# Kernel optimization log

Hardware: AMD Instinct MI355X
Metric: run time of the kernel (lower is better)

Reference implementation:

```python
import jax, jax.numpy as jnp
import numpy as np

NUM_ENTITIES = 100000
NUM_RELATIONS = 1000
ENTITY_DIM = 256
RELATION_DIM = 256
BATCH = 8192


def setup_inputs() -> dict:
    key = jax.random.key(0)
    k1, k2, k3, k4, k5, k6 = jax.random.split(key, 6)
    bound_e = 6.0 / np.sqrt(ENTITY_DIM)
    bound_r = 6.0 / np.sqrt(RELATION_DIM)
    entity_embed = jax.random.uniform(k1, (NUM_ENTITIES, ENTITY_DIM), jnp.float32, -bound_e, bound_e)
    relation_embed = jax.random.uniform(k2, (NUM_RELATIONS, RELATION_DIM), jnp.float32, -bound_r, bound_r)
    # proj matrices initialized near identity (TransR convention) plus small noise
    eye = jnp.broadcast_to(jnp.eye(RELATION_DIM, ENTITY_DIM, dtype=jnp.float32), (NUM_RELATIONS, RELATION_DIM, ENTITY_DIM))
    proj = (eye + 0.01 * jax.random.normal(k3, (NUM_RELATIONS, RELATION_DIM, ENTITY_DIM), jnp.float32)).reshape(NUM_RELATIONS, RELATION_DIM * ENTITY_DIM)
    h = jax.random.randint(k4, (BATCH,), 0, NUM_ENTITIES)
    r = jax.random.randint(k5, (BATCH,), 0, NUM_RELATIONS)
    t = jax.random.randint(k6, (BATCH,), 0, NUM_ENTITIES)
    return {"h": h, "r": r, "t": t, "entity_embed": entity_embed,
            "relation_embed": relation_embed, "proj": proj}


def reference(h, r, t, entity_embed, relation_embed, proj) -> jnp.ndarray:
    # gather embeddings
    h_emb = entity_embed[h]                      # [B, ed]
    t_emb = entity_embed[t]                      # [B, ed]
    r_emb = relation_embed[r]                    # [B, rd]
    M = proj[r].reshape(-1, RELATION_DIM, ENTITY_DIM)  # [B, rd, ed]
    # batched matvec: project head/tail into relation space
    h_r = jnp.einsum('bre,be->br', M, h_emb)     # [B, rd]
    t_r = jnp.einsum('bre,be->br', M, t_emb)     # [B, rd]
    diff = h_r + r_emb - t_r
    return -jnp.sqrt(jnp.sum(diff * diff, axis=-1))  # [B]
```

## Files before the change

kernel.cpp:

```cpp
#include <hip/hip_runtime.h>
#include <math.h>


#define ED   256
#define TR64 64
#define NT   4
#define CAP  64

typedef __attribute__((ext_vector_type(8))) short bf16x8;
typedef __attribute__((ext_vector_type(4))) float f32x4;

__device__ __forceinline__ unsigned int bfbits_rne(float x) {
    unsigned int u = __builtin_bit_cast(unsigned int, x);
    return (u + 0x7fffu + ((u >> 16) & 1u)) >> 16;
}
__device__ __forceinline__ unsigned int pack2(float x, float y) {
    return bfbits_rne(x) | (bfbits_rne(y) << 16);
}

__global__ void transr_prep_kernel(const int* __restrict__ h, const int* __restrict__ r,
                                   const int* __restrict__ t, const float* __restrict__ ent,
                                   int B, int nbCsr,
                                   int* __restrict__ counts, int* __restrict__ itemsG,
                                   uint4* __restrict__ Dbf)
{
    const int tid = threadIdx.x;
    if ((int)blockIdx.x < nbCsr) {
        int i = blockIdx.x * 256 + tid;
        if (i < B) {
            int rv  = r[i];
            int pos = atomicAdd(&counts[rv], 1);
            if (pos < CAP) itemsG[rv * CAP + pos] = i;
        }
    } else {
        int i = ((int)blockIdx.x - nbCsr) * 256 + tid;
        if (i < B * 32) {
            int b = i >> 5, c = i & 31;
            const float4* hv = (const float4*)ent + (size_t)h[b] * 64 + c * 2;
            const float4* tv = (const float4*)ent + (size_t)t[b] * 64 + c * 2;
            float4 a0 = hv[0], a1 = hv[1], b0 = tv[0], b1 = tv[1];
            uint4 o;
            o.x = pack2(a0.x - b0.x, a0.y - b0.y);
            o.y = pack2(a0.z - b0.z, a0.w - b0.w);
            o.z = pack2(a1.x - b1.x, a1.y - b1.y);
            o.w = pack2(a1.z - b1.z, a1.w - b1.w);
            Dbf[i] = o;
        }
    }
}

__global__ __launch_bounds__(256, 2)
void transr_mfma_kernel(const float* __restrict__ rel, const float* __restrict__ proj,
                        const int* __restrict__ counts, const int* __restrict__ itemsG,
                        const uint4* __restrict__ Dbf, float* __restrict__ part)
{
    __shared__ __align__(16) unsigned short Mt[TR64 * ED];
    __shared__ __align__(16) unsigned short Dt[16 * ED];
    __shared__ float remb_s[TR64];
    __shared__ float sacc[4][16];
    __shared__ int   items_s[CAP];

    const int relid = blockIdx.x;
    const int tile  = blockIdx.y;
    const int tid   = threadIdx.x;

    const int n = min(counts[relid], CAP);
    if (n == 0) return;

    if (tid < CAP) items_s[tid] = (tid < n) ? itemsG[relid * CAP + tid] : 0;
    if (tid < TR64) remb_s[tid] = rel[(size_t)relid * ED + tile * TR64 + tid];

    {
        const float4* Mg4 = (const float4*)(proj + (size_t)relid * ED * ED
                                                 + (size_t)tile * TR64 * ED);
        #pragma unroll
        for (int it = 0; it < 8; ++it) {
            int f  = tid + 256 * it;
            int rr = f >> 5, c = f & 31;
            float4 a = Mg4[2 * f], b = Mg4[2 * f + 1];
            uint4 o;
            o.x = pack2(a.x, a.y); o.y = pack2(a.z, a.w);
            o.z = pack2(b.x, b.y); o.w = pack2(b.z, b.w);
            *(uint4*)&Mt[rr * ED + ((c ^ (rr & 7)) << 3)] = o;
        }
    }

    const int l  = tid & 63;
    const int w  = tid >> 6;
    const int li = l & 15;
    const int lk = l >> 4;
    const int arow = w * 16 + li;
    const int aswz = arow & 7, bswz = li & 7;

    for (int c0 = 0; c0 < n; c0 += 16) {
        #pragma unroll
        for (int it = 0; it < 2; ++it) {
            int f = tid + 256 * it;
            int j = f >> 5, c = f & 31;
            uint4 v = {0u, 0u, 0u, 0u};
            if (c0 + j < n) v = Dbf[(size_t)items_s[c0 + j] * 32 + c];
            *(uint4*)&Dt[j * ED + ((c ^ (j & 7)) << 3)] = v;
        }
        __syncthreads();

        f32x4 acc = {0.f, 0.f, 0.f, 0.f};
        #pragma unroll
        for (int kk = 0; kk < 8; ++kk) {
            int c = kk * 4 + lk;
            bf16x8 av = *(const bf16x8*)&Mt[arow * ED + ((c ^ aswz) << 3)];
            bf16x8 bv = *(const bf16x8*)&Dt[li * ED + ((c ^ bswz) << 3)];
            acc = __builtin_amdgcn_mfma_f32_16x16x32_bf16(av, bv, acc, 0, 0, 0);
        }

        float s = 0.f;
        #pragma unroll
        for (int j = 0; j < 4; ++j) {
            float v = acc[j] + remb_s[w * 16 + lk * 4 + j];
            s = fmaf(v, v, s);
        }
        s += __shfl_xor(s, 16);
        s += __shfl_xor(s, 32);
        if (l < 16) sacc[w][l] = s;
        __syncthreads();

        if (tid < 16 && c0 + tid < n) {
            part[(size_t)items_s[c0 + tid] * NT + tile] =
                sacc[0][tid] + sacc[1][tid] + sacc[2][tid] + sacc[3][tid];
        }
    }
}

__global__ void transr_finalize_kernel(const float* __restrict__ part,
                                       float* __restrict__ out, int B)
{
    int i = blockIdx.x * 256 + threadIdx.x;
    if (i < B) {
        float4 p = *(const float4*)(part + (size_t)i * NT);
        out[i] = -sqrtf(p.x + p.y + p.z + p.w);
    }
}

#define FNCH 16
#define FCAP 2048
__global__ __launch_bounds__(256, 1)
void transr_score_kernel(const int* __restrict__ h, const int* __restrict__ r,
                         const int* __restrict__ t, const float* __restrict__ ent,
                         const float* __restrict__ rel, const float* __restrict__ proj,
                         float* __restrict__ out, int B)
{
    __shared__ int   items[FCAP];
    __shared__ int   s_n;
    __shared__ __align__(16) float D[FNCH][ED];
    __shared__ __align__(16) float Mt2[32][ED];
    __shared__ float remb[ED];
    __shared__ float sacc2[FNCH];

    const int relid = blockIdx.x;
    const int tid   = threadIdx.x;
    if (tid == 0) s_n = 0;
    __syncthreads();

    for (int i0 = tid * 4; i0 < B; i0 += 256 * 4) {
        int4 rv = *(const int4*)(r + i0);
        if (rv.x == relid) { int p = atomicAdd(&s_n, 1); if (p < FCAP) items[p] = i0;     }
        if (rv.y == relid) { int p = atomicAdd(&s_n, 1); if (p < FCAP) items[p] = i0 + 1; }
        if (rv.z == relid) { int p = atomicAdd(&s_n, 1); if (p < FCAP) items[p] = i0 + 2; }
        if (rv.w == relid) { int p = atomicAdd(&s_n, 1); if (p < FCAP) items[p] = i0 + 3; }
    }
    remb[tid] = rel[(size_t)relid * ED + tid];
    __syncthreads();

    int n = s_n < FCAP ? s_n : FCAP;
    if (n == 0) return;

    const float* Mg = proj + (size_t)relid * (ED * ED);
    const int rt = tid & 31, g = tid >> 5, sw = rt & 7;

    for (int c0 = 0; c0 < n; c0 += FNCH) {
        const int nc = min(FNCH, n - c0);
        {
            const int j  = tid >> 4;
            const int e4 = tid & 15;
            if (j < nc) {
                const int b = items[c0 + j];
                const float4* hv = (const float4*)(ent + (size_t)h[b] * ED);
                const float4* tv = (const float4*)(ent + (size_t)t[b] * ED);
                #pragma unroll
                for (int k = 0; k < 4; ++k) {
                    float4 a = hv[e4 + 16 * k];
                    float4 c = tv[e4 + 16 * k];
                    float4 d4; d4.x = a.x - c.x; d4.y = a.y - c.y;
                               d4.z = a.z - c.z; d4.w = a.w - c.w;
                    *(float4*)&D[j][4 * (e4 + 16 * k)] = d4;
                }
            } else {
                float4 z; z.x = z.y = z.z = z.w = 0.f;
                #pragma unroll
                for (int k = 0; k < 4; ++k) *(float4*)&D[j][4 * (e4 + 16 * k)] = z;
            }
        }
        __syncthreads();

        float sq0 = 0.f, sq1 = 0.f;
        for (int tile = 0; tile < 8; ++tile) {
            const float4* Mg4 = (const float4*)(Mg + (size_t)tile * 32 * ED);
            #pragma unroll
            for (int k = 0; k < 8; ++k) {
                int f = tid + 256 * k;
                int rr = f >> 6, e4 = f & 63;
                *(float4*)&Mt2[rr][4 * (e4 ^ (rr & 7))] = Mg4[f];
            }
            __syncthreads();

            float acc0 = 0.f, acc1 = 0.f;
            #pragma unroll 8
            for (int e4 = 0; e4 < 64; ++e4) {
                float4 m  = *(const float4*)&Mt2[rt][4 * (e4 ^ sw)];
                float4 d0 = *(const float4*)&D[g][4 * e4];
                float4 d1 = *(const float4*)&D[g + 8][4 * e4];
                acc0 = fmaf(m.x, d0.x, acc0); acc0 = fmaf(m.y, d0.y, acc0);
                acc0 = fmaf(m.z, d0.z, acc0); acc0 = fmaf(m.w, d0.w, acc0);
                acc1 = fmaf(m.x, d1.x, acc1); acc1 = fmaf(m.y, d1.y, acc1);
                acc1 = fmaf(m.z, d1.z, acc1); acc1 = fmaf(m.w, d1.w, acc1);
            }
            const float rb = remb[tile * 32 + rt];
            float s0 = acc0 + rb; s0 *= s0;
            float s1 = acc1 + rb; s1 *= s1;
            #pragma unroll
            for (int off = 16; off >= 1; off >>= 1) {
                s0 += __shfl_xor(s0, off, 32);
                s1 += __shfl_xor(s1, off, 32);
            }
            sq0 += s0; sq1 += s1;
            __syncthreads();
        }
        if (rt == 0) { sacc2[g] = sq0; sacc2[g + 8] = sq1; }
        __syncthreads();
        if (tid < nc) out[items[c0 + tid]] = -sqrtf(sacc2[tid]);
        __syncthreads();
    }
}

extern "C" void kernel_launch(void* const* d_in, const int* in_sizes, int n_in,
                              void* d_out, int out_size, void* d_ws, size_t ws_size,
                              hipStream_t stream)
{
    const int*   h    = (const int*)d_in[0];
    const int*   r    = (const int*)d_in[1];
    const int*   t    = (const int*)d_in[2];
    const float* ent  = (const float*)d_in[3];
    const float* rel  = (const float*)d_in[4];
    const float* proj = (const float*)d_in[5];
    float*       out  = (float*)d_out;

    const int B  = in_sizes[0];
    const int NR = in_sizes[5] / (ED * ED);

    size_t o_counts = 0;
    size_t o_items  = (o_counts + (size_t)NR * 4 + 255) & ~(size_t)255;
    size_t o_part   = (o_items + (size_t)NR * CAP * 4 + 255) & ~(size_t)255;
    size_t o_D      = (o_part + (size_t)B * NT * 4 + 255) & ~(size_t)255;
    size_t need     = o_D + (size_t)B * ED * 2;

    if (ws_size >= need) {
        int*   counts = (int*)((char*)d_ws + o_counts);
        int*   itemsG = (int*)((char*)d_ws + o_items);
        float* part   = (float*)((char*)d_ws + o_part);
        uint4* Dbf    = (uint4*)((char*)d_ws + o_D);

        hipMemsetAsync(counts, 0, (size_t)NR * 4, stream);

        const int nbCsr = (B + 255) / 256;
        const int nbD   = (B * 32 + 255) / 256;
        transr_prep_kernel<<<nbCsr + nbD, 256, 0, stream>>>(h, r, t, ent, B, nbCsr,
                                                            counts, itemsG, Dbf);
        transr_mfma_kernel<<<dim3(NR, NT), 256, 0, stream>>>(rel, proj, counts,
                                                             itemsG, Dbf, part);
        transr_finalize_kernel<<<(B + 255) / 256, 256, 0, stream>>>(part, out, B);
    } else {
        transr_score_kernel<<<NR, 256, 0, stream>>>(h, r, t, ent, rel, proj, out, B);
    }
}
```

Measured before the change: 62.97 us.

## Bucket batch items per relation in-block and read D directly from global

Drops the memset and the global atomic CSR bucketing. Each MFMA block now scans the whole r array itself and collects its relation's items in shared memory. The B operand is loaded straight from global memory instead of being staged in LDS, which removes the per-chunk syncthreads. Per-wave partial sums are written out and reduced in finalize, and occupancy rises to 4 blocks per CU. The cost is that each of the NR*NT blocks reads all of r (redundant traffic) and the partial buffer grows fourfold.

```diff
diff --git a/kernel.cpp b/kernel.cpp
--- a/kernel.cpp
+++ b/kernel.cpp
@@ -18,57 +18,52 @@
     return bfbits_rne(x) | (bfbits_rne(y) << 16);
 }
 
-__global__ void transr_prep_kernel(const int* __restrict__ h, const int* __restrict__ r,
-                                   const int* __restrict__ t, const float* __restrict__ ent,
-                                   int B, int nbCsr,
-                                   int* __restrict__ counts, int* __restrict__ itemsG,
+__global__ void transr_prep_kernel(const int* __restrict__ h, const int* __restrict__ t,
+                                   const float* __restrict__ ent, int B,
                                    uint4* __restrict__ Dbf)
 {
-    const int tid = threadIdx.x;
-    if ((int)blockIdx.x < nbCsr) {
-        int i = blockIdx.x * 256 + tid;
-        if (i < B) {
-            int rv  = r[i];
-            int pos = atomicAdd(&counts[rv], 1);
-            if (pos < CAP) itemsG[rv * CAP + pos] = i;
-        }
-    } else {
-        int i = ((int)blockIdx.x - nbCsr) * 256 + tid;
-        if (i < B * 32) {
-            int b = i >> 5, c = i & 31;
-            const float4* hv = (const float4*)ent + (size_t)h[b] * 64 + c * 2;
-            const float4* tv = (const float4*)ent + (size_t)t[b] * 64 + c * 2;
-            float4 a0 = hv[0], a1 = hv[1], b0 = tv[0], b1 = tv[1];
-            uint4 o;
-            o.x = pack2(a0.x - b0.x, a0.y - b0.y);
-            o.y = pack2(a0.z - b0.z, a0.w - b0.w);
-            o.z = pack2(a1.x - b1.x, a1.y - b1.y);
-            o.w = pack2(a1.z - b1.z, a1.w - b1.w);
-            Dbf[i] = o;
-        }
-    }
-}
-
-__global__ __launch_bounds__(256, 2)
-void transr_mfma_kernel(const float* __restrict__ rel, const float* __restrict__ proj,
-                        const int* __restrict__ counts, const int* __restrict__ itemsG,
-                        const uint4* __restrict__ Dbf, float* __restrict__ part)
+    int i = blockIdx.x * 256 + threadIdx.x;
+    if (i < B * 32) {
+        int b = i >> 5, c = i & 31;
+        const float4* hv = (const float4*)ent + (size_t)h[b] * 64 + c * 2;
+        const float4* tv = (const float4*)ent + (size_t)t[b] * 64 + c * 2;
+        float4 a0 = hv[0], a1 = hv[1], b0 = tv[0], b1 = tv[1];
+        uint4 o;
+        o.x = pack2(a0.x - b0.x, a0.y - b0.y);
+        o.y = pack2(a0.z - b0.z, a0.w - b0.w);
+        o.z = pack2(a1.x - b1.x, a1.y - b1.y);
+        o.w = pack2(a1.z - b1.z, a1.w - b1.w);
+        Dbf[i] = o;
+    }
+}
+
+__global__ __launch_bounds__(256, 4)
+void transr_mfma_kernel(const int* __restrict__ r, const float* __restrict__ rel,
+                        const float* __restrict__ proj, const uint4* __restrict__ Dbf,
+                        float* __restrict__ part, int B)
 {
     __shared__ __align__(16) unsigned short Mt[TR64 * ED];
-    __shared__ __align__(16) unsigned short Dt[16 * ED];
-    __shared__ float remb_s[TR64];
-    __shared__ float sacc[4][16];
-    __shared__ int   items_s[CAP];
+    __shared__ int items_s[CAP];
+    __shared__ int s_n;
 
     const int relid = blockIdx.x;
     const int tile  = blockIdx.y;
     const int tid   = threadIdx.x;
 
-    const int n = min(counts[relid], CAP);
+    if (tid == 0) s_n = 0;
+    __syncthreads();
+
+    for (int i0 = tid * 4; i0 < B; i0 += 1024) {
+        int4 rv = *(const int4*)(r + i0);
+        if (rv.x == relid) { int p = atomicAdd(&s_n, 1); if (p < CAP) items_s[p] = i0;     }
+        if (rv.y == relid) { int p = atomicAdd(&s_n, 1); if (p < CAP) items_s[p] = i0 + 1; }
+        if (rv.z == relid) { int p = atomicAdd(&s_n, 1); if (p < CAP) items_s[p] = i0 + 2; }
+        if (rv.w == relid) { int p = atomicAdd(&s_n, 1); if (p < CAP) items_s[p] = i0 + 3; }
+    }
+    __syncthreads();
+
+    const int n = min(s_n, CAP);
     if (n == 0) return;
-
-    if (tid < CAP) items_s[tid] = (tid < n) ? itemsG[relid * CAP + tid] : 0;
-    if (tid < TR64) remb_s[tid] = rel[(size_t)relid * ED + tile * TR64 + tid];
 
     {
         const float4* Mg4 = (const float4*)(proj + (size_t)relid * ED * ED
@@ -85,48 +80,40 @@
         }
     }
 
-    const int l  = tid & 63;
-    const int w  = tid >> 6;
-    const int li = l & 15;
-    const int lk = l >> 4;
+    const int l    = tid & 63;
+    const int w    = tid >> 6;
+    const int li   = l & 15;
+    const int lk   = l >> 4;
     const int arow = w * 16 + li;
-    const int aswz = arow & 7, bswz = li & 7;
+    const int aswz = arow & 7;
+
+    f32x4 rbv = *(const f32x4*)(rel + (size_t)relid * ED + tile * TR64 + w * 16 + lk * 4);
+
+    __syncthreads();
 
     for (int c0 = 0; c0 < n; c0 += 16) {
-        #pragma unroll
-        for (int it = 0; it < 2; ++it) {
-            int f = tid + 256 * it;
-            int j = f >> 5, c = f & 31;
-            uint4 v = {0u, 0u, 0u, 0u};
-            if (c0 + j < n) v = Dbf[(size_t)items_s[c0 + j] * 32 + c];
-            *(uint4*)&Dt[j * ED + ((c ^ (j & 7)) << 3)] = v;
-        }
-        __syncthreads();
+        const int bslot = min(c0 + li, n - 1);
+        const uint4* bbase = Dbf + (size_t)items_s[bslot] * 32;
 
         f32x4 acc = {0.f, 0.f, 0.f, 0.f};
         #pragma unroll
         for (int kk = 0; kk < 8; ++kk) {
             int c = kk * 4 + lk;
             bf16x8 av = *(const bf16x8*)&Mt[arow * ED + ((c ^ aswz) << 3)];
-            bf16x8 bv = *(const bf16x8*)&Dt[li * ED + ((c ^ bswz) << 3)];
+            bf16x8 bv = __builtin_bit_cast(bf16x8, bbase[c]);
             acc = __builtin_amdgcn_mfma_f32_16x16x32_bf16(av, bv, acc, 0, 0, 0);
         }
 
         float s = 0.f;
         #pragma unroll
         for (int j = 0; j < 4; ++j) {
-            float v = acc[j] + remb_s[w * 16 + lk * 4 + j];
+            float v = acc[j] + rbv[j];
             s = fmaf(v, v, s);
         }
         s += __shfl_xor(s, 16);
         s += __shfl_xor(s, 32);
-        if (l < 16) sacc[w][l] = s;
-        __syncthreads();
-
-        if (tid < 16 && c0 + tid < n) {
-            part[(size_t)items_s[c0 + tid] * NT + tile] =
-                sacc[0][tid] + sacc[1][tid] + sacc[2][tid] + sacc[3][tid];
-        }
+        if (lk == 0 && c0 + li < n)
+            part[(size_t)items_s[c0 + li] * 16 + tile * 4 + w] = s;
     }
 }
 
@@ -135,8 +122,13 @@
 {
     int i = blockIdx.x * 256 + threadIdx.x;
     if (i < B) {
-        float4 p = *(const float4*)(part + (size_t)i * NT);
-        out[i] = -sqrtf(p.x + p.y + p.z + p.w);
+        const float4* p = (const float4*)(part + (size_t)i * 16);
+        float4 a = p[0], b = p[1], c = p[2], d = p[3];
+        float s = a.x + a.y + a.z + a.w;
+        s += b.x + b.y + b.z + b.w;
+        s += c.x + c.y + c.z + c.w;
+        s += d.x + d.y + d.z + d.w;
+        out[i] = -sqrtf(s);
     }
 }
 
@@ -256,26 +248,16 @@
     const int B  = in_sizes[0];
     const int NR = in_sizes[5] / (ED * ED);
 
-    size_t o_counts = 0;
-    size_t o_items  = (o_counts + (size_t)NR * 4 + 255) & ~(size_t)255;
-    size_t o_part   = (o_items + (size_t)NR * CAP * 4 + 255) & ~(size_t)255;
-    size_t o_D      = (o_part + (size_t)B * NT * 4 + 255) & ~(size_t)255;
-    size_t need     = o_D + (size_t)B * ED * 2;
+    size_t o_part = 0;
+    size_t o_D    = (o_part + (size_t)B * 16 * 4 + 255) & ~(size_t)255;
+    size_t need   = o_D + (size_t)B * ED * 2;
 
     if (ws_size >= need) {
-        int*   counts = (int*)((char*)d_ws + o_counts);
-        int*   itemsG = (int*)((char*)d_ws + o_items);
-        float* part   = (float*)((char*)d_ws + o_part);
-        uint4* Dbf    = (uint4*)((char*)d_ws + o_D);
-
-        hipMemsetAsync(counts, 0, (size_t)NR * 4, stream);
-
-        const int nbCsr = (B + 255) / 256;
-        const int nbD   = (B * 32 + 255) / 256;
-        transr_prep_kernel<<<nbCsr + nbD, 256, 0, stream>>>(h, r, t, ent, B, nbCsr,
-                                                            counts, itemsG, Dbf);
-        transr_mfma_kernel<<<dim3(NR, NT), 256, 0, stream>>>(rel, proj, counts,
-                                                             itemsG, Dbf, part);
+        float* part = (float*)((char*)d_ws + o_part);
+        uint4* Dbf  = (uint4*)((char*)d_ws + o_D);
+
+        transr_prep_kernel<<<(B * 32 + 255) / 256, 256, 0, stream>>>(h, t, ent, B, Dbf);
+        transr_mfma_kernel<<<dim3(NR, NT), 256, 0, stream>>>(r, rel, proj, Dbf, part, B);
         transr_finalize_kernel<<<(B + 255) / 256, 256, 0, stream>>>(part, out, B);
     } else {
         transr_score_kernel<<<NR, 256, 0, stream>>>(h, r, t, ent, rel, proj, out, B);
```

Result: no change. 64.18 us (+1.9%).
